# Optimization experiments

Measured on AMD Instinct MI355X. Metric: run time of the kernel, lower is better.

The kernel has to match this reference:

```python
import jax, jax.numpy as jnp
import numpy as np

N, E, B = 50000, 1600000, 64
VOCAB, EMB = 1000, 16
HID, OUT_FEAT = 192, 128   # hidden_sf*model_dim, out_sf*output_channels
MODEL_DIM, DEMO, OUT_DIM = 64, 5, 2
EPS = 1e-7  # GENConv eps


def setup_inputs() -> dict:
    key = jax.random.key(0)
    ks = jax.random.split(key, 18)
    f32 = jnp.float32

    def rn(k, shape, scale):
        return jax.random.normal(k, shape, dtype=f32) * scale

    node_idx = jax.random.randint(ks[0], (N,), 0, VOCAB)
    edge_index = jax.random.randint(ks[1], (2, E), 0, N)
    batch = jnp.sort(jax.random.randint(ks[2], (N,), 0, B))
    demographics = rn(ks[3], (B, DEMO), 1.0)

    emb = rn(ks[4], (VOCAB, EMB), 1.0)
    dims = [(EMB, HID), (HID, HID), (HID, HID), (HID, OUT_FEAT)]
    params = {}
    for i, (din, dout) in enumerate(dims):
        params[f"W{i}"] = rn(ks[5 + 2 * i], (din, dout), 1.0 / np.sqrt(din))
        params[f"b{i}"] = jnp.zeros((dout,), f32)
    params["Wc1"] = rn(ks[13], (OUT_FEAT + DEMO, MODEL_DIM), 1.0 / np.sqrt(OUT_FEAT + DEMO))
    params["bc1"] = jnp.zeros((MODEL_DIM,), f32)
    params["Wc2"] = rn(ks[14], (MODEL_DIM, OUT_DIM), 1.0 / np.sqrt(MODEL_DIM))
    params["bc2"] = jnp.zeros((OUT_DIM,), f32)

    return {"node_idx": node_idx, "edge_index": edge_index, "batch": batch,
            "demographics": demographics, "emb": emb, **params}


def _gen_conv(x, src, dst, W, b):
    # GENConv (num_layers=1, aggr='add', edge_attr=None):
    #   out_i = Linear( sum_{j->i} (relu(x_j) + eps) + x_i )
    m = jax.nn.relu(x) + EPS                                   # [N, D]
    agg = jax.ops.segment_sum(m[src], dst, num_segments=x.shape[0])
    return (agg + x) @ W + b


def reference(node_idx, edge_index, batch, demographics, emb,
              W0, b0, W1, b1, W2, b2, W3, b3, Wc1, bc1, Wc2, bc2):
    x = emb[node_idx]                                          # [N, 16]
    src, dst = edge_index[0], edge_index[1]
    for W, b in ((W0, b0), (W1, b1), (W2, b2), (W3, b3)):
        x = _gen_conv(x, src, dst, W, b)                       # [N, D_l]
    # global_mean_pool
    cnt = jax.ops.segment_sum(jnp.ones((x.shape[0],), x.dtype), batch, num_segments=B)
    g = jax.ops.segment_sum(x, batch, num_segments=B) / jnp.maximum(cnt, 1.0)[:, None]
    feats = jnp.concatenate([g, demographics], axis=1)         # [B, 133]
    h = jax.nn.relu(feats @ Wc1 + bc1)                         # dropout = identity (eval)
    return h @ Wc2 + bc2                                       # [B, out_dim]
```

## Files before the change

kernel.cpp:

```cpp
#include <hip/hip_runtime.h>
#include <stdint.h>

#define EPS 1e-7f

constexpr int N_NODES = 50000;
constexpr int N_EDGES = 1600000;
constexpr int BATCH = 64;
constexpr int EMB = 16;
constexpr int HID = 192;
constexpr int OUTF = 128;
constexpr int DEMO = 5;
constexpr int MODEL_DIM = 64;
constexpr int OUT_DIM = 2;

constexpr int NPART = 8;
constexpr int PART_NODES = (N_NODES + NPART - 1) / NPART;

constexpr int NBKT = 16;
constexpr int BKT_DIV = (N_NODES + NBKT - 1) / NBKT;
constexpr int NB2 = N_NODES * NBKT;

constexpr int SCAN2_CHUNK = 1024;
constexpr int NCHUNK2 = (NB2 + SCAN2_CHUNK - 1) / SCAN2_CHUNK;

typedef unsigned short bf16_t;
typedef short s8v __attribute__((ext_vector_type(8)));
typedef float f4v __attribute__((ext_vector_type(4)));

static __device__ __forceinline__ float bf2f(bf16_t u) {
  return __uint_as_float(((uint32_t)u) << 16);
}
static __device__ __forceinline__ bf16_t f2bf(float f) {
  uint32_t b = __float_as_uint(f);
  return (bf16_t)((b + 0x7FFFu + ((b >> 16) & 1u)) >> 16);
}

__global__ void emb_gather(const int* __restrict__ idx, const float* __restrict__ emb,
                           bf16_t* __restrict__ x) {
  int t = blockIdx.x * blockDim.x + threadIdx.x;
  if (t >= N_NODES * EMB) return;
  int node = t / EMB, f = t % EMB;
  x[t] = f2bf(emb[idx[node] * EMB + f]);
}

__global__ void hist2_kernel(const int* __restrict__ src, const int* __restrict__ dst,
                             int* __restrict__ hist2) {
  int part = blockIdx.x & (NPART - 1);
  int blk = blockIdx.x >> 3;
  int nthread = (gridDim.x >> 3) * blockDim.x;
  int lo = part * PART_NODES, hi = lo + PART_NODES;
  for (int e = blk * blockDim.x + threadIdx.x; e < N_EDGES; e += nthread) {
    int d = dst[e];
    if (d >= lo && d < hi) atomicAdd(&hist2[d * NBKT + src[e] / BKT_DIV], 1);
  }
}

__global__ void chunk_sum2_kernel(const int* __restrict__ hist2, int* __restrict__ chunk_sum) {
  int t = threadIdx.x;
  int base = blockIdx.x * SCAN2_CHUNK + t * 4;
  int v = 0;
#pragma unroll
  for (int j = 0; j < 4; ++j) {
    int i = base + j;
    if (i < NB2) v += hist2[i];
  }
#pragma unroll
  for (int off = 32; off > 0; off >>= 1) v += __shfl_down(v, off);
  __shared__ int s[4];
  if ((t & 63) == 0) s[t >> 6] = v;
  __syncthreads();
  if (t == 0) chunk_sum[blockIdx.x] = s[0] + s[1] + s[2] + s[3];
}

__global__ void scan_chunks2_kernel(const int* __restrict__ chunk_sum,
                                    int* __restrict__ chunk_off) {
  __shared__ int s[1024];
  int t = threadIdx.x;
  int v = (t < NCHUNK2) ? chunk_sum[t] : 0;
  s[t] = v;
  __syncthreads();
  for (int off = 1; off < 1024; off <<= 1) {
    int u = (t >= off) ? s[t - off] : 0;
    __syncthreads();
    s[t] += u;
    __syncthreads();
  }
  if (t < NCHUNK2) chunk_off[t] = s[t] - v;
}

__global__ void chunk_scan_write2_kernel(const int* __restrict__ hist2,
                                         const int* __restrict__ chunk_off,
                                         int* __restrict__ cursor2,
                                         int* __restrict__ row_start) {
  __shared__ int s[256];
  int t = threadIdx.x;
  int base = blockIdx.x * SCAN2_CHUNK + t * 4;
  int local[4];
  int tsum = 0;
#pragma unroll
  for (int j = 0; j < 4; ++j) {
    int i = base + j;
    local[j] = (i < NB2) ? hist2[i] : 0;
    tsum += local[j];
  }
  s[t] = tsum;
  __syncthreads();
  for (int off = 1; off < 256; off <<= 1) {
    int u = (t >= off) ? s[t - off] : 0;
    __syncthreads();
    s[t] += u;
    __syncthreads();
  }
  int run = chunk_off[blockIdx.x] + s[t] - tsum;
#pragma unroll
  for (int j = 0; j < 4; ++j) {
    int i = base + j;
    if (i < NB2) {
      cursor2[i] = run;
      if ((i & (NBKT - 1)) == 0) row_start[i / NBKT] = run;
      if (i == NB2 - 1) row_start[N_NODES] = run + local[j];
      run += local[j];
    }
  }
}

__global__ void scatter_kernel(const int* __restrict__ src, const int* __restrict__ dst,
                               int* __restrict__ cursor2, int* __restrict__ csr_src) {
  int part = blockIdx.x & (NPART - 1);
  int blk = blockIdx.x >> 3;
  int nthread = (gridDim.x >> 3) * blockDim.x;
  int lo = part * PART_NODES, hi = lo + PART_NODES;
  for (int e = blk * blockDim.x + threadIdx.x; e < N_EDGES; e += nthread) {
    int d = dst[e];
    if (d >= lo && d < hi) {
      int s = src[e];
      int pos = atomicAdd(&cursor2[d * NBKT + s / BKT_DIV], 1);
      csr_src[pos] = s;
    }
  }
}

template <int TPN, int NPB>
__global__ void agg2_kernel(const uint32_t* __restrict__ x, const int* __restrict__ row_start,
                            const int* __restrict__ csr_src, uint32_t* __restrict__ out) {
  int f = threadIdx.x % TPN;
  int node = blockIdx.x * NPB + threadIdx.x / TPN;
  if (node >= N_NODES) return;
  int s0 = row_start[node], s1 = row_start[node + 1];
  float deps = (float)(s1 - s0) * EPS;
  uint32_t xv = x[(size_t)node * TPN + f];
  float a0 = __uint_as_float(xv << 16) + deps;
  float a1 = __uint_as_float(xv & 0xFFFF0000u) + deps;
  int e = s0;
  for (; e + 8 <= s1; e += 8) {
    int idx[8];
#pragma unroll
    for (int j = 0; j < 8; ++j) idx[j] = csr_src[e + j];
    uint32_t v[8];
#pragma unroll
    for (int j = 0; j < 8; ++j) v[j] = x[(size_t)idx[j] * TPN + f];
#pragma unroll
    for (int j = 0; j < 8; ++j) {
      a0 += fmaxf(__uint_as_float(v[j] << 16), 0.f);
      a1 += fmaxf(__uint_as_float(v[j] & 0xFFFF0000u), 0.f);
    }
  }
  for (; e < s1; ++e) {
    uint32_t v = x[(size_t)csr_src[e] * TPN + f];
    a0 += fmaxf(__uint_as_float(v << 16), 0.f);
    a1 += fmaxf(__uint_as_float(v & 0xFFFF0000u), 0.f);
  }
  out[(size_t)node * TPN + f] = (uint32_t)f2bf(a0) | ((uint32_t)f2bf(a1) << 16);
}

__global__ void wprep_kernel(const float* __restrict__ W, int K, int NOUT,
                             bf16_t* __restrict__ Wt) {
  int t = blockIdx.x * blockDim.x + threadIdx.x;
  if (t >= K * NOUT) return;
  int k = t / NOUT, n = t % NOUT;
  Wt[(size_t)n * K + k] = f2bf(W[t]);
}

constexpr int FU_TPN = 24;
constexpr int FU_NPB = 16;
constexpr int FU_LDR = 200;
template <int NOUT, bool OUT_BF16>
__global__ void fused_agg_gemm(const uint4* __restrict__ x, const int* __restrict__ row_start,
                               const int* __restrict__ csr_src,
                               const bf16_t* __restrict__ Wt, const float* __restrict__ bias,
                               void* __restrict__ outp) {
  constexpr int K = 192;
  constexpr int ROW = 24;
  __shared__ bf16_t tile[FU_NPB * FU_LDR];

  {
    int f = threadIdx.x % FU_TPN;
    int ln = threadIdx.x / FU_TPN;
    int node = blockIdx.x * FU_NPB + ln;
    int s0 = row_start[node], s1 = row_start[node + 1];
    float deps = (float)(s1 - s0) * EPS;
    uint4 xv = x[(size_t)node * ROW + f];
    float a[8];
    {
      uint32_t pk[4] = {xv.x, xv.y, xv.z, xv.w};
#pragma unroll
      for (int q = 0; q < 4; ++q) {
        a[2 * q]     = __uint_as_float(pk[q] << 16) + deps;
        a[2 * q + 1] = __uint_as_float(pk[q] & 0xFFFF0000u) + deps;
      }
    }
    int e = s0;
    for (; e + 4 <= s1; e += 4) {
      int idx[4];
#pragma unroll
      for (int j = 0; j < 4; ++j) idx[j] = csr_src[e + j];
      uint4 v[4];
#pragma unroll
      for (int j = 0; j < 4; ++j) v[j] = x[(size_t)idx[j] * ROW + f];
#pragma unroll
      for (int j = 0; j < 4; ++j) {
        uint32_t pk[4] = {v[j].x, v[j].y, v[j].z, v[j].w};
#pragma unroll
        for (int q = 0; q < 4; ++q) {
          a[2 * q]     += fmaxf(__uint_as_float(pk[q] << 16), 0.f);
          a[2 * q + 1] += fmaxf(__uint_as_float(pk[q] & 0xFFFF0000u), 0.f);
        }
      }
    }
    for (; e < s1; ++e) {
      uint4 v = x[(size_t)csr_src[e] * ROW + f];
      uint32_t pk[4] = {v.x, v.y, v.z, v.w};
#pragma unroll
      for (int q = 0; q < 4; ++q) {
        a[2 * q]     += fmaxf(__uint_as_float(pk[q] << 16), 0.f);
        a[2 * q + 1] += fmaxf(__uint_as_float(pk[q] & 0xFFFF0000u), 0.f);
      }
    }
    uint4 o;
    o.x = (uint32_t)f2bf(a[0]) | ((uint32_t)f2bf(a[1]) << 16);
    o.y = (uint32_t)f2bf(a[2]) | ((uint32_t)f2bf(a[3]) << 16);
    o.z = (uint32_t)f2bf(a[4]) | ((uint32_t)f2bf(a[5]) << 16);
    o.w = (uint32_t)f2bf(a[6]) | ((uint32_t)f2bf(a[7]) << 16);
    *reinterpret_cast<uint4*>(&tile[ln * FU_LDR + f * 8]) = o;
  }
  __syncthreads();

  {
    constexpr int KT = K / 32;
    constexpr int NT = NOUT / 16;
    int wave = threadIdx.x >> 6;
    int lane = threadIdx.x & 63;
    int rlo = lane & 15;
    int kbase = (lane >> 4) * 8;

    s8v af[KT];
#pragma unroll
    for (int kt = 0; kt < KT; ++kt)
      af[kt] = *reinterpret_cast<const s8v*>(&tile[rlo * FU_LDR + kbase + kt * 32]);

    int r0 = (lane >> 4) * 4;
    for (int nt = wave; nt < NT; nt += 6) {
      const bf16_t* wp = Wt + ((size_t)(nt * 16 + rlo)) * K + kbase;
      f4v c = {0.f, 0.f, 0.f, 0.f};
#pragma unroll
      for (int kt = 0; kt < KT; ++kt) {
        s8v b = *(const s8v*)(wp + kt * 32);
        c = __builtin_amdgcn_mfma_f32_16x16x32_bf16(af[kt], b, c, 0, 0, 0);
      }
      int col = nt * 16 + rlo;
      float bv = bias[col];
#pragma unroll
      for (int r = 0; r < 4; ++r) {
        float v = c[r] + bv;
        size_t o = (size_t)(blockIdx.x * FU_NPB + r0 + r) * NOUT + col;
        if constexpr (OUT_BF16) ((bf16_t*)outp)[o] = f2bf(v);
        else                    ((float*)outp)[o] = v;
      }
    }
  }
}

template <int DIN, int DOUT, bool OUT_BF16>
__global__ void gemm_kernel(const bf16_t* __restrict__ in, const float* __restrict__ W,
                            const float* __restrict__ bias, void* __restrict__ outp) {
  constexpr int ROWS = 16;
  __shared__ bf16_t tile[ROWS * DIN];
  int c = threadIdx.x;
  int base = blockIdx.x * ROWS;

  {
    const uint4* gsrc = reinterpret_cast<const uint4*>(in + (size_t)base * DIN);
    uint4* ldst = reinterpret_cast<uint4*>(tile);
    constexpr int NV = ROWS * DIN * 2 / 16;
    for (int i = threadIdx.x; i < NV; i += blockDim.x) ldst[i] = gsrc[i];
  }
  __syncthreads();

  float acc[ROWS];
  float bc = bias[c];
#pragma unroll
  for (int r = 0; r < ROWS; ++r) acc[r] = bc;

  for (int k0 = 0; k0 < DIN; k0 += 8) {
    float w[8];
#pragma unroll
    for (int j = 0; j < 8; ++j) w[j] = W[(size_t)(k0 + j) * DOUT + c];
#pragma unroll
    for (int r = 0; r < ROWS; ++r) {
      uint4 packed = *reinterpret_cast<const uint4*>(&tile[r * DIN + k0]);
      uint32_t pk[4] = {packed.x, packed.y, packed.z, packed.w};
#pragma unroll
      for (int q = 0; q < 4; ++q) {
        float lo = __uint_as_float(pk[q] << 16);
        float hi = __uint_as_float(pk[q] & 0xFFFF0000u);
        acc[r] = fmaf(lo, w[2 * q], acc[r]);
        acc[r] = fmaf(hi, w[2 * q + 1], acc[r]);
      }
    }
  }

#pragma unroll
  for (int r = 0; r < ROWS; ++r) {
    size_t o = (size_t)(base + r) * DOUT + c;
    if constexpr (OUT_BF16) ((bf16_t*)outp)[o] = f2bf(acc[r]);
    else                    ((float*)outp)[o] = acc[r];
  }
}

constexpr int POOL_CHUNK = 100;
__global__ void pool_kernel(const float* __restrict__ x, const int* __restrict__ batch,
                            float* __restrict__ gsum, int* __restrict__ gcnt) {
  int f = threadIdx.x;
  int start = blockIdx.x * POOL_CHUNK;
  if (start >= N_NODES) return;
  int end = min(start + POOL_CHUNK, N_NODES);
  int cur = batch[start];
  float acc = 0.f;
  int cnt = 0;
  for (int i = start; i < end; ++i) {
    int b = batch[i];
    if (b != cur) {
      atomicAdd(&gsum[cur * OUTF + f], acc);
      if (f == 0) atomicAdd(&gcnt[cur], cnt);
      acc = 0.f; cnt = 0; cur = b;
    }
    acc += x[(size_t)i * OUTF + f];
    cnt++;
  }
  atomicAdd(&gsum[cur * OUTF + f], acc);
  if (f == 0) atomicAdd(&gcnt[cur], cnt);
}

__global__ void mlp_kernel(const float* __restrict__ gsum, const int* __restrict__ gcnt,
                           const float* __restrict__ demo,
                           const float* __restrict__ Wc1, const float* __restrict__ bc1,
                           const float* __restrict__ Wc2, const float* __restrict__ bc2,
                           float* __restrict__ out) {
  int b = blockIdx.x;
  int c = threadIdx.x;
  __shared__ float feats[OUTF + DEMO];
  float inv = 1.f / fmaxf((float)gcnt[b], 1.f);
  for (int k = c; k < OUTF; k += MODEL_DIM) feats[k] = gsum[b * OUTF + k] * inv;
  if (c < DEMO) feats[OUTF + c] = demo[b * DEMO + c];
  __syncthreads();
  float s = bc1[c];
#pragma unroll
  for (int k = 0; k < OUTF + DEMO; ++k) s = fmaf(feats[k], Wc1[k * MODEL_DIM + c], s);
  float h = fmaxf(s, 0.f);
  float o0 = h * Wc2[c * OUT_DIM + 0];
  float o1 = h * Wc2[c * OUT_DIM + 1];
#pragma unroll
  for (int off = 32; off > 0; off >>= 1) {
    o0 += __shfl_down(o0, off);
    o1 += __shfl_down(o1, off);
  }
  if (c == 0) {
    out[b * OUT_DIM + 0] = o0 + bc2[0];
    out[b * OUT_DIM + 1] = o1 + bc2[1];
  }
}

extern "C" void kernel_launch(void* const* d_in, const int* in_sizes, int n_in,
                              void* d_out, int out_size, void* d_ws, size_t ws_size,
                              hipStream_t stream) {
  const int*   node_idx = (const int*)d_in[0];
  const int*   edge_index = (const int*)d_in[1];
  const int*   batch = (const int*)d_in[2];
  const float* demo = (const float*)d_in[3];
  const float* emb  = (const float*)d_in[4];
  const float* W0 = (const float*)d_in[5];  const float* b0 = (const float*)d_in[6];
  const float* W1 = (const float*)d_in[7];  const float* b1 = (const float*)d_in[8];
  const float* W2 = (const float*)d_in[9];  const float* b2 = (const float*)d_in[10];
  const float* W3 = (const float*)d_in[11]; const float* b3 = (const float*)d_in[12];
  const float* Wc1 = (const float*)d_in[13]; const float* bc1 = (const float*)d_in[14];
  const float* Wc2 = (const float*)d_in[15]; const float* bc2 = (const float*)d_in[16];
  const int* src = edge_index;
  const int* dst = edge_index + N_EDGES;
  float* out = (float*)d_out;

  char* ws = (char*)d_ws;
  size_t off = 0;
  auto alloc = [&](size_t bytes) {
    void* p = ws + off;
    off += (bytes + 255) & ~size_t(255);
    return p;
  };
  bf16_t* xbf     = (bf16_t*)alloc((size_t)N_NODES * HID * 2);
  bf16_t* xbf2    = (bf16_t*)alloc((size_t)N_NODES * HID * 2);
  bf16_t* xbf0    = (bf16_t*)alloc((size_t)N_NODES * EMB * 2);
  bf16_t* agg0    = (bf16_t*)alloc((size_t)N_NODES * EMB * 2);
  float*  x3      = (float*)alloc((size_t)N_NODES * OUTF * 4);
  int*   csr_src  = (int*)alloc((size_t)N_EDGES * 4);
  int*   hist2    = (int*)alloc((size_t)NB2 * 4);
  int*   cursor2  = (int*)alloc((size_t)NB2 * 4);
  int*   row_start= (int*)alloc((size_t)(N_NODES + 1) * 4);
  int*   chunk_sum= (int*)alloc((size_t)NCHUNK2 * 4);
  int*   chunk_off= (int*)alloc((size_t)NCHUNK2 * 4);
  float* gsum     = (float*)alloc((size_t)BATCH * OUTF * 4);
  int*   gcnt     = (int*)alloc((size_t)BATCH * 4);
  bf16_t* Wt1     = (bf16_t*)alloc((size_t)HID * HID * 2);
  bf16_t* Wt2     = (bf16_t*)alloc((size_t)HID * HID * 2);
  bf16_t* Wt3     = (bf16_t*)alloc((size_t)OUTF * HID * 2);

  hipMemsetAsync(hist2, 0, (size_t)NB2 * 4, stream);
  hipMemsetAsync(gsum, 0, (size_t)BATCH * OUTF * 4, stream);
  hipMemsetAsync(gcnt, 0, (size_t)BATCH * 4, stream);

  wprep_kernel<<<(HID * HID + 255) / 256, 256, 0, stream>>>(W1, HID, HID, Wt1);
  wprep_kernel<<<(HID * HID + 255) / 256, 256, 0, stream>>>(W2, HID, HID, Wt2);
  wprep_kernel<<<(HID * OUTF + 255) / 256, 256, 0, stream>>>(W3, HID, OUTF, Wt3);

  hist2_kernel<<<NPART * 256, 256, 0, stream>>>(src, dst, hist2);
  chunk_sum2_kernel<<<NCHUNK2, 256, 0, stream>>>(hist2, chunk_sum);
  scan_chunks2_kernel<<<1, 1024, 0, stream>>>(chunk_sum, chunk_off);
  chunk_scan_write2_kernel<<<NCHUNK2, 256, 0, stream>>>(hist2, chunk_off, cursor2, row_start);
  scatter_kernel<<<NPART * 256, 256, 0, stream>>>(src, dst, cursor2, csr_src);

  constexpr int FU_GRID = N_NODES / FU_NPB;

  emb_gather<<<(N_NODES * EMB + 255) / 256, 256, 0, stream>>>(node_idx, emb, xbf0);
  agg2_kernel<8, 32><<<(N_NODES + 31) / 32, 256, 0, stream>>>(
      (const uint32_t*)xbf0, row_start, csr_src, (uint32_t*)agg0);
  gemm_kernel<16, 192, true><<<N_NODES / 16, 192, 0, stream>>>(agg0, W0, b0, xbf);
  fused_agg_gemm<192, true><<<FU_GRID, FU_TPN * FU_NPB, 0, stream>>>(
      (const uint4*)xbf, row_start, csr_src, Wt1, b1, xbf2);
  fused_agg_gemm<192, true><<<FU_GRID, FU_TPN * FU_NPB, 0, stream>>>(
      (const uint4*)xbf2, row_start, csr_src, Wt2, b2, xbf);
  fused_agg_gemm<128, false><<<FU_GRID, FU_TPN * FU_NPB, 0, stream>>>(
      (const uint4*)xbf, row_start, csr_src, Wt3, b3, x3);

  pool_kernel<<<(N_NODES + POOL_CHUNK - 1) / POOL_CHUNK, OUTF, 0, stream>>>(x3, batch, gsum, gcnt);
  mlp_kernel<<<BATCH, MODEL_DIM, 0, stream>>>(gsum, gcnt, demo, Wc1, bc1, Wc2, bc2, out);
}
```

Before: 501.6 us.

## Pre-bin edges by destination partition before histogram and scatter passes

```diff
diff --git a/kernel.cpp b/kernel.cpp
--- a/kernel.cpp
+++ b/kernel.cpp
@@ -15,6 +15,7 @@
 
 constexpr int NPART = 8;
 constexpr int PART_NODES = (N_NODES + NPART - 1) / NPART;
+constexpr int PCAP = 204800;
 
 constexpr int NBKT = 16;
 constexpr int BKT_DIV = (N_NODES + NBKT - 1) / NBKT;
@@ -22,6 +23,11 @@
 
 constexpr int SCAN2_CHUNK = 1024;
 constexpr int NCHUNK2 = (NB2 + SCAN2_CHUNK - 1) / SCAN2_CHUNK;
+
+constexpr int EP_THREADS = 256;
+constexpr int EP_EPT = 8;
+constexpr int EP_EPB = EP_THREADS * EP_EPT;
+constexpr int EP_GRID = (N_EDGES + EP_EPB - 1) / EP_EPB;
 
 typedef unsigned short bf16_t;
 typedef short s8v __attribute__((ext_vector_type(8)));
@@ -43,15 +49,54 @@
   x[t] = f2bf(emb[idx[node] * EMB + f]);
 }
 
-__global__ void hist2_kernel(const int* __restrict__ src, const int* __restrict__ dst,
-                             int* __restrict__ hist2) {
+__global__ void init_gcur_kernel(int* __restrict__ gcur) {
+  int t = threadIdx.x;
+  if (t < NPART) gcur[t] = t * PCAP;
+}
+
+__global__ void epart_kernel(const int* __restrict__ src, const int* __restrict__ dst,
+                             int* __restrict__ gcur, int2* __restrict__ epart) {
+  __shared__ int cur[NPART];
+  __shared__ int base[NPART];
+  int t = threadIdx.x;
+  if (t < NPART) cur[t] = 0;
+  __syncthreads();
+  int e0 = blockIdx.x * EP_EPB;
+  int s[EP_EPT], d[EP_EPT], p[EP_EPT], loc[EP_EPT];
+#pragma unroll
+  for (int j = 0; j < EP_EPT; ++j) {
+    int e = e0 + t + j * EP_THREADS;
+    if (e < N_EDGES) {
+      s[j] = src[e];
+      d[j] = dst[e];
+      p[j] = d[j] / PART_NODES;
+      loc[j] = atomicAdd(&cur[p[j]], 1);
+    } else {
+      p[j] = -1;
+    }
+  }
+  __syncthreads();
+  if (t < NPART) base[t] = atomicAdd(&gcur[t], cur[t]);
+  __syncthreads();
+#pragma unroll
+  for (int j = 0; j < EP_EPT; ++j) {
+    if (p[j] >= 0) {
+      int2 v;
+      v.x = s[j]; v.y = d[j];
+      epart[base[p[j]] + loc[j]] = v;
+    }
+  }
+}
+
+__global__ void hist2b_kernel(const int2* __restrict__ epart, const int* __restrict__ gcur,
+                              int* __restrict__ hist2) {
   int part = blockIdx.x & (NPART - 1);
   int blk = blockIdx.x >> 3;
   int nthread = (gridDim.x >> 3) * blockDim.x;
-  int lo = part * PART_NODES, hi = lo + PART_NODES;
-  for (int e = blk * blockDim.x + threadIdx.x; e < N_EDGES; e += nthread) {
-    int d = dst[e];
-    if (d >= lo && d < hi) atomicAdd(&hist2[d * NBKT + src[e] / BKT_DIV], 1);
+  int end = gcur[part];
+  for (int e = part * PCAP + blk * blockDim.x + threadIdx.x; e < end; e += nthread) {
+    int2 v = epart[e];
+    atomicAdd(&hist2[v.y * NBKT + v.x / BKT_DIV], 1);
   }
 }
 
@@ -124,19 +169,16 @@
   }
 }
 
-__global__ void scatter_kernel(const int* __restrict__ src, const int* __restrict__ dst,
-                               int* __restrict__ cursor2, int* __restrict__ csr_src) {
+__global__ void scatter2b_kernel(const int2* __restrict__ epart, const int* __restrict__ gcur,
+                                 int* __restrict__ cursor2, int* __restrict__ csr_src) {
   int part = blockIdx.x & (NPART - 1);
   int blk = blockIdx.x >> 3;
   int nthread = (gridDim.x >> 3) * blockDim.x;
-  int lo = part * PART_NODES, hi = lo + PART_NODES;
-  for (int e = blk * blockDim.x + threadIdx.x; e < N_EDGES; e += nthread) {
-    int d = dst[e];
-    if (d >= lo && d < hi) {
-      int s = src[e];
-      int pos = atomicAdd(&cursor2[d * NBKT + s / BKT_DIV], 1);
-      csr_src[pos] = s;
-    }
+  int end = gcur[part];
+  for (int e = part * PCAP + blk * blockDim.x + threadIdx.x; e < end; e += nthread) {
+    int2 v = epart[e];
+    int pos = atomicAdd(&cursor2[v.y * NBKT + v.x / BKT_DIV], 1);
+    csr_src[pos] = v.x;
   }
 }
 
@@ -411,6 +453,8 @@
   bf16_t* agg0    = (bf16_t*)alloc((size_t)N_NODES * EMB * 2);
   float*  x3      = (float*)alloc((size_t)N_NODES * OUTF * 4);
   int*   csr_src  = (int*)alloc((size_t)N_EDGES * 4);
+  int2*  epart    = (int2*)alloc((size_t)NPART * PCAP * 8);
+  int*   gcur     = (int*)alloc((size_t)NPART * 4);
   int*   hist2    = (int*)alloc((size_t)NB2 * 4);
   int*   cursor2  = (int*)alloc((size_t)NB2 * 4);
   int*   row_start= (int*)alloc((size_t)(N_NODES + 1) * 4);
@@ -430,11 +474,13 @@
   wprep_kernel<<<(HID * HID + 255) / 256, 256, 0, stream>>>(W2, HID, HID, Wt2);
   wprep_kernel<<<(HID * OUTF + 255) / 256, 256, 0, stream>>>(W3, HID, OUTF, Wt3);
 
-  hist2_kernel<<<NPART * 256, 256, 0, stream>>>(src, dst, hist2);
+  init_gcur_kernel<<<1, NPART, 0, stream>>>(gcur);
+  epart_kernel<<<EP_GRID, EP_THREADS, 0, stream>>>(src, dst, gcur, epart);
+  hist2b_kernel<<<NPART * 96, 256, 0, stream>>>(epart, gcur, hist2);
   chunk_sum2_kernel<<<NCHUNK2, 256, 0, stream>>>(hist2, chunk_sum);
   scan_chunks2_kernel<<<1, 1024, 0, stream>>>(chunk_sum, chunk_off);
   chunk_scan_write2_kernel<<<NCHUNK2, 256, 0, stream>>>(hist2, chunk_off, cursor2, row_start);
-  scatter_kernel<<<NPART * 256, 256, 0, stream>>>(src, dst, cursor2, csr_src);
+  scatter2b_kernel<<<NPART * 96, 256, 0, stream>>>(epart, gcur, cursor2, csr_src);
 
   constexpr int FU_GRID = N_NODES / FU_NPB;
 
```

Result: slower. 516.7 us (+3.0%).
